# Performance work log

Hardware: AMD Instinct MI355X
Metric: run time of the kernel (lower is better)

## Reference

```python
import jax, jax.numpy as jnp
import numpy as np

B, SQ, ST, SI = 8, 4096, 77, 16
C, DC, H = 1280, 2048, 20
DH = C // H  # 64
SCALE = 1.0 / np.sqrt(DH).astype(np.float32)
SCALE_ID = 1.0
SCALE_HAIR = 1.0


def setup_inputs() -> dict:
    key = jax.random.key(0)
    ks = jax.random.split(key, 12)
    std = 0.02
    return {
        "hidden_states": jax.random.normal(ks[0], (B, SQ, C), jnp.float32),
        "text_states": jax.random.normal(ks[1], (B, ST, DC), jnp.float32),
        "id_states": jax.random.normal(ks[2], (B, SI, DC), jnp.float32),
        "hair_states": jax.random.normal(ks[3], (B, SI, DC), jnp.float32),
        # weights stored as [in, out] (transpose of torch nn.Linear layout)
        "Wq": jax.random.normal(ks[4], (C, C), jnp.float32) * std,
        "Wk": jax.random.normal(ks[5], (DC, C), jnp.float32) * std,
        "Wv": jax.random.normal(ks[6], (DC, C), jnp.float32) * std,
        "Wo": jax.random.normal(ks[7], (C, C), jnp.float32) * std,
        "b_o": jnp.zeros((C,), jnp.float32),
        "Wk_id": jax.random.normal(ks[8], (DC, C), jnp.float32) * std,
        "Wv_id": jax.random.normal(ks[9], (DC, C), jnp.float32) * std,
        "Wk_hair": jax.random.normal(ks[10], (DC, C), jnp.float32) * std,
        "Wv_hair": jax.random.normal(ks[11], (DC, C), jnp.float32) * std,
    }


def _heads(x):
    # [B, S, C] -> [B, H, S, DH]
    b, s, _ = x.shape
    return x.reshape(b, s, H, DH).transpose(0, 2, 1, 3)


def _merge(x):
    # [B, H, S, DH] -> [B, S, C]
    b, h, s, d = x.shape
    return x.transpose(0, 2, 1, 3).reshape(b, s, h * d)


def _attend(q, k, v):
    # q: [B,H,Sq,DH], k/v: [B,H,Sk,DH]; fp32 scores (attn_fp32=True)
    scores = jnp.einsum("bhqd,bhkd->bhqk", q.astype(jnp.float32), k.astype(jnp.float32)) * SCALE
    p = jax.nn.softmax(scores, axis=-1)
    return jnp.einsum("bhqk,bhkd->bhqd", p, v.astype(jnp.float32))


def reference(hidden_states, text_states, id_states, hair_states, Wq, Wk, Wv, Wo, b_o, Wk_id, Wv_id, Wk_hair, Wv_hair):
    q = _heads(hidden_states @ Wq)
    # base cross-attention to text (standard diffusers AttnProcessor)
    base = _attend(q, _heads(text_states @ Wk), _heads(text_states @ Wv))
    result = _merge(base) @ Wo + b_o
    # ID branch: own K/V projections, shared query and to_out
    out_id = _attend(q, _heads(id_states @ Wk_id), _heads(id_states @ Wv_id))
    result = result + SCALE_ID * (_merge(out_id) @ Wo + b_o)
    # hair branch
    out_h = _attend(q, _heads(hair_states @ Wk_hair), _heads(hair_states @ Wv_hair))
    result = result + SCALE_HAIR * (_merge(out_h) @ Wo + b_o)
    return result
```

## Files before the change

### kernel.cpp

```cpp
#include <hip/hip_runtime.h>
#include <cstdint>
#include <cstddef>

typedef unsigned short u16;
typedef __attribute__((ext_vector_type(4))) float     f32x4_t;
typedef __attribute__((ext_vector_type(8))) __bf16    bf16x8_t;
typedef __attribute__((ext_vector_type(8))) u16       u16x8_t;
typedef __attribute__((ext_vector_type(4))) u16       u16x4_t;
typedef __attribute__((ext_vector_type(4))) float     fvec4_t;

#define DEVI __device__ __forceinline__

constexpr int Bn  = 8;
constexpr int SQn = 4096;
constexpr int STn = 77;
constexpr int SIn = 16;
constexpr int Cn  = 1280;
constexpr int DCn = 2048;
constexpr int Hn  = 20;
constexpr float SCALEf = 0.125f;
constexpr float L2E    = 1.4426950408889634f;

typedef const __attribute__((address_space(1))) void* gas_t;
typedef __attribute__((address_space(3))) void*       las_t;

DEVI u16 f2bf(float f) {
  union { float f; unsigned u; } cv; cv.f = f;
  unsigned u = cv.u;
  return (u16)((u + 0x7FFFu + ((u >> 16) & 1u)) >> 16);
}

__global__ __launch_bounds__(256) void cast_bf16_kernel(
    const float* __restrict__ src, u16* __restrict__ dst, int n8) {
  int i = blockIdx.x * 256 + threadIdx.x;
  if (i >= n8) return;
  const fvec4_t* s4 = (const fvec4_t*)src;
  fvec4_t a = s4[2 * i], b = s4[2 * i + 1];
  u16x8_t o;
  o[0] = f2bf(a[0]); o[1] = f2bf(a[1]); o[2] = f2bf(a[2]); o[3] = f2bf(a[3]);
  o[4] = f2bf(b[0]); o[5] = f2bf(b[1]); o[6] = f2bf(b[2]); o[7] = f2bf(b[3]);
  ((u16x8_t*)dst)[i] = o;
}

struct TrArgs {
  const float* src[8];
  u16*         dst[8];
  int          Kd[8];
};

__global__ __launch_bounds__(256) void transpose_cast_kernel(TrArgs ta) {
  int z = blockIdx.z;
  int K = ta.Kd[z];
  int k0 = blockIdx.x * 32;
  if (k0 >= K) return;
  int n0 = blockIdx.y * 32;
  __shared__ float tile[32][33];
  int tx = threadIdx.x & 31, ty = threadIdx.x >> 5;
  const float* src = ta.src[z];
#pragma unroll
  for (int i = 0; i < 4; i++) {
    int r = ty + 8 * i;
    tile[r][tx] = src[(size_t)(k0 + r) * Cn + n0 + tx];
  }
  __syncthreads();
  u16* dst = ta.dst[z];
#pragma unroll
  for (int i = 0; i < 4; i++) {
    int r = ty + 8 * i;
    dst[(size_t)(n0 + r) * K + k0 + tx] = f2bf(tile[tx][r]);
  }
}

template <int OUT_MODE, int A_HM>
__global__ __launch_bounds__(512, 2) void gemm256_kernel(
    const u16* __restrict__ A, const u16* __restrict__ Bt,
    void* __restrict__ Cout, const float* __restrict__ bias, int M, int K) {
  __shared__ __align__(16) u16 lds[2][2][256 * 64];
  const int t = threadIdx.x;
  const int w = t >> 6, l = t & 63;
  const int wr = w >> 2, wc = w & 3;
  const int lr = l & 15;
  const int m0 = blockIdx.x * 256, n0 = blockIdx.y * 256;
  const int NT = K >> 6;

  f32x4_t acc[8][4];
#pragma unroll
  for (int am = 0; am < 8; am++)
#pragma unroll
    for (int an = 0; an < 4; an++) {
      f32x4_t z = {0.f, 0.f, 0.f, 0.f};
      acc[am][an] = z;
    }

  auto stagePart = [&](int cb, int kt, int i) {
    const int k0 = kt * 64;
    int row = i * 64 + w * 8 + (l >> 3);
    int col16 = (l & 7) ^ (row & 7);
    const u16* ga;
    if (A_HM) {
      int gr = m0 + row, bb = gr >> 12, ss = gr & 4095;
      ga = A + (((size_t)bb * Hn + kt) * SQn + ss) * 64 + col16 * 8;
    } else {
      ga = A + (size_t)(m0 + row) * K + k0 + col16 * 8;
    }
    __builtin_amdgcn_global_load_lds((gas_t)ga, (las_t)(&lds[cb][0][0] + (size_t)(i * 512 + w * 64) * 8), 16, 0, 0);
    const u16* gb = Bt + (size_t)(n0 + row) * K + k0 + col16 * 8;
    __builtin_amdgcn_global_load_lds((gas_t)gb, (las_t)(&lds[cb][1][0] + (size_t)(i * 512 + w * 64) * 8), 16, 0, 0);
  };
  auto readB = [&](bf16x8_t (&dst)[2][2], const u16* bB, int qn) {
#pragma unroll
    for (int n = 0; n < 2; n++) {
      int row = wc * 64 + qn * 32 + n * 16 + lr;
#pragma unroll
      for (int kk = 0; kk < 2; kk++) {
        int slot = kk * 4 + (l >> 4);
        dst[n][kk] = *(const bf16x8_t*)&bB[row * 64 + ((slot ^ (row & 7)) * 8)];
      }
    }
  };
  auto readA = [&](bf16x8_t (&dst)[4][2], const u16* bA, int qm) {
#pragma unroll
    for (int m = 0; m < 4; m++) {
      int row = wr * 128 + qm * 64 + m * 16 + lr;
#pragma unroll
      for (int kk = 0; kk < 2; kk++) {
        int slot = kk * 4 + (l >> 4);
        dst[m][kk] = *(const bf16x8_t*)&bA[row * 64 + ((slot ^ (row & 7)) * 8)];
      }
    }
  };
  auto mfma16 = [&](bf16x8_t (&Af)[4][2], bf16x8_t (&Bf)[2][2], int qm, int qn) {
    __builtin_amdgcn_s_setprio(1);
#pragma unroll
    for (int m = 0; m < 4; m++)
#pragma unroll
      for (int n = 0; n < 2; n++) {
        acc[qm * 4 + m][qn * 2 + n] = __builtin_amdgcn_mfma_f32_16x16x32_bf16(
            Af[m][0], Bf[n][0], acc[qm * 4 + m][qn * 2 + n], 0, 0, 0);
        acc[qm * 4 + m][qn * 2 + n] = __builtin_amdgcn_mfma_f32_16x16x32_bf16(
            Af[m][1], Bf[n][1], acc[qm * 4 + m][qn * 2 + n], 0, 0, 0);
      }
    __builtin_amdgcn_s_setprio(0);
  };

#pragma unroll
  for (int i = 0; i < 4; i++) stagePart(0, 0, i);
#pragma unroll
  for (int i = 0; i < 4; i++) stagePart(1, 1, i);
  asm volatile("s_waitcnt vmcnt(8)" ::: "memory");
  __builtin_amdgcn_sched_barrier(0);
  __builtin_amdgcn_s_barrier();

  for (int kt = 0; kt < NT; kt++) {
    const int cb = kt & 1;
    const u16* bA = &lds[cb][0][0];
    const u16* bB = &lds[cb][1][0];
    const bool st = (kt + 2 < NT);
    bf16x8_t Ar[4][2], B0[2][2], B1[2][2];

    readB(B0, bB, 0);
    readA(Ar, bA, 0);
    __builtin_amdgcn_s_barrier();
    asm volatile("s_waitcnt lgkmcnt(0)" ::: "memory");
    __builtin_amdgcn_sched_barrier(0);
    mfma16(Ar, B0, 0, 0);
    __builtin_amdgcn_s_barrier();

    readB(B1, bB, 1);
    __builtin_amdgcn_s_barrier();
    asm volatile("s_waitcnt lgkmcnt(0)" ::: "memory");
    __builtin_amdgcn_sched_barrier(0);
    mfma16(Ar, B1, 0, 1);
    __builtin_amdgcn_s_barrier();

    readA(Ar, bA, 1);
    __builtin_amdgcn_s_barrier();
    if (st) { stagePart(cb, kt + 2, 0); stagePart(cb, kt + 2, 1); }
    asm volatile("s_waitcnt lgkmcnt(0)" ::: "memory");
    __builtin_amdgcn_sched_barrier(0);
    mfma16(Ar, B0, 1, 0);
    __builtin_amdgcn_s_barrier();

    if (st) { stagePart(cb, kt + 2, 2); stagePart(cb, kt + 2, 3); }
    mfma16(Ar, B1, 1, 1);

    if (st) {
      asm volatile("s_waitcnt vmcnt(8)" ::: "memory");
    } else if (kt + 1 < NT) {
      asm volatile("s_waitcnt vmcnt(0)" ::: "memory");
    }
    __builtin_amdgcn_sched_barrier(0);
    __builtin_amdgcn_s_barrier();
  }

#pragma unroll
  for (int am = 0; am < 8; am++) {
    int rbase = m0 + wr * 128 + am * 16 + (l >> 4) * 4;
#pragma unroll
    for (int an = 0; an < 4; an++) {
      int col = n0 + wc * 64 + an * 16 + lr;
#pragma unroll
      for (int j = 0; j < 4; j++) {
        int r = rbase + j;
        if (OUT_MODE == 1) {
          ((float*)Cout)[(size_t)r * Cn + col] = acc[am][an][j] + 3.0f * bias[col];
        } else {
          int bb = r >> 12, ss = r & 4095;
          int hh = (n0 >> 6) + wc, dd = an * 16 + lr;
          ((u16*)Cout)[(((size_t)bb * Hn + hh) * SQn + ss) * 64 + dd] = f2bf(acc[am][an][j]);
        }
      }
    }
  }
}

DEVI void gemm_body(const u16* __restrict__ A, const u16* __restrict__ Bt,
                    u16* __restrict__ Cout, int M, int S, int K, int mtile, int ntile) {
  __shared__ __align__(16) u16 lA[128 * 64];
  __shared__ __align__(16) u16 lB[128 * 64];
  const int t = threadIdx.x;
  const int w = t >> 6, l = t & 63;
  const int wr = w >> 1, wc = w & 1;
  const int m0 = mtile * 128, n0 = ntile * 128;
  const int lr = l & 15, lk = (l >> 4) * 8;

  f32x4_t acc[4][4];
#pragma unroll
  for (int m = 0; m < 4; m++)
#pragma unroll
    for (int n = 0; n < 4; n++) {
      f32x4_t z = {0.f, 0.f, 0.f, 0.f};
      acc[m][n] = z;
    }

  for (int k0 = 0; k0 < K; k0 += 64) {
    __syncthreads();
#pragma unroll
    for (int i = 0; i < 4; i++) {
      int c = i * 256 + t;
      int row = c >> 3, ch = c & 7;
      int rA = m0 + row;
      rA = rA < M ? rA : M - 1;
      const u16* ga = A + (size_t)rA * K + k0 + ch * 8;
      __builtin_amdgcn_global_load_lds((gas_t)ga, (las_t)&lA[(i * 256 + w * 64) * 8], 16, 0, 0);
      const u16* gb = Bt + (size_t)(n0 + row) * K + k0 + ch * 8;
      __builtin_amdgcn_global_load_lds((gas_t)gb, (las_t)&lB[(i * 256 + w * 64) * 8], 16, 0, 0);
    }
    __syncthreads();
#pragma unroll
    for (int kk = 0; kk < 2; kk++) {
      bf16x8_t af[4], bf[4];
#pragma unroll
      for (int m = 0; m < 4; m++)
        af[m] = *(const bf16x8_t*)&lA[(64 * wr + 16 * m + lr) * 64 + kk * 32 + lk];
#pragma unroll
      for (int n = 0; n < 4; n++)
        bf[n] = *(const bf16x8_t*)&lB[(64 * wc + 16 * n + lr) * 64 + kk * 32 + lk];
#pragma unroll
      for (int m = 0; m < 4; m++)
#pragma unroll
        for (int n = 0; n < 4; n++)
          acc[m][n] = __builtin_amdgcn_mfma_f32_16x16x32_bf16(af[m], bf[n], acc[m][n], 0, 0, 0);
    }
  }

  const int rj = (l >> 4) * 4;
  const int hh = ntile * 2 + wc;
#pragma unroll
  for (int m = 0; m < 4; m++) {
    int rbase = m0 + 64 * wr + 16 * m + rj;
#pragma unroll
    for (int n = 0; n < 4; n++) {
      int dd = 16 * n + lr;
#pragma unroll
      for (int j = 0; j < 4; j++) {
        int r = rbase + j;
        if (r < M) {
          int bb = r / S, ss = r - bb * S;
          Cout[(((size_t)bb * Hn + hh) * S + ss) * 64 + dd] = f2bf(acc[m][n][j]);
        }
      }
    }
  }
}

struct KV6 {
  const u16* A[6];
  const u16* Bt[6];
  u16*       Cp[6];
  int        M[6];
  int        S[6];
};

__global__ __launch_bounds__(256) void gemm_kv_kernel(KV6 kv) {
  int z = blockIdx.z;
  int M = kv.M[z];
  if ((int)blockIdx.x * 128 >= M) return;
  gemm_body(kv.A[z], kv.Bt[z], kv.Cp[z], M, kv.S[z], DCn, blockIdx.x, blockIdx.y);
}

__global__ __launch_bounds__(256) void attn_kernel(
    const u16* __restrict__ q,
    const u16* __restrict__ ktx, const u16* __restrict__ vtx,
    const u16* __restrict__ kid, const u16* __restrict__ vid,
    const u16* __restrict__ kh,  const u16* __restrict__ vh,
    u16* __restrict__ osum) {
  __shared__ __align__(16) u16 KP[4 * 16 * 136];
  __shared__ __align__(16) u16 Vt[64 * 128];

  const int t = threadIdx.x, w = t >> 6, l = t & 63;
  const int bh = blockIdx.y;
  const int lr = l & 15, lk = (l >> 4) * 8;

  const u16* qB   = q   + ((size_t)bh) * SQn * 64;
  const u16* ktxB = ktx + ((size_t)bh) * STn * 64;
  const u16* vtxB = vtx + ((size_t)bh) * STn * 64;
  const u16* kidB = kid + ((size_t)bh) * SIn * 64;
  const u16* vidB = vid + ((size_t)bh) * SIn * 64;
  const u16* khB  = kh  + ((size_t)bh) * SIn * 64;
  const u16* vhB  = vh  + ((size_t)bh) * SIn * 64;
  u16*       oB   = osum + ((size_t)bh) * SQn * 64;

  for (int i = t; i < 112 * 8; i += 256) {
    int row = i >> 3, ch = i & 7;
    u16x8_t vv;
#pragma unroll
    for (int x = 0; x < 8; x++) vv[x] = 0;
    if (row < 77)
      vv = *(const u16x8_t*)(ktxB + (size_t)row * 64 + ch * 8);
    else if (row >= 80 && row < 96)
      vv = *(const u16x8_t*)(kidB + (size_t)(row - 80) * 64 + ch * 8);
    else if (row >= 96)
      vv = *(const u16x8_t*)(khB + (size_t)(row - 96) * 64 + ch * 8);
    *(u16x8_t*)&KP[row * 72 + ch * 8] = vv;
  }
  for (int i = t; i < 128 * 8; i += 256) {
    int key = i >> 3, ch = i & 7;
    u16x8_t vv;
#pragma unroll
    for (int x = 0; x < 8; x++) vv[x] = 0;
    if (key < 77)
      vv = *(const u16x8_t*)(vtxB + (size_t)key * 64 + ch * 8);
    else if (key >= 80 && key < 96)
      vv = *(const u16x8_t*)(vidB + (size_t)(key - 80) * 64 + ch * 8);
    else if (key >= 96 && key < 112)
      vv = *(const u16x8_t*)(vhB + (size_t)(key - 96) * 64 + ch * 8);
    int G = key >> 3, wk = key & 7;
#pragma unroll
    for (int x = 0; x < 8; x++) {
      int d = ch * 8 + x;
      int Gs = G ^ x ^ ch;
      Vt[d * 128 + Gs * 8 + wk] = vv[x];
    }
  }
  __syncthreads();

  bf16x8_t kf[7][2];
#pragma unroll
  for (int tt = 0; tt < 7; tt++)
#pragma unroll
    for (int kk = 0; kk < 2; kk++)
      kf[tt][kk] = *(const bf16x8_t*)&KP[(tt * 16 + lr) * 72 + kk * 32 + lk];
  __syncthreads();

  u16* Pw = &KP[w * 16 * 136];
  {
    u16x4_t z4; z4[0] = 0; z4[1] = 0; z4[2] = 0; z4[3] = 0;
    *(u16x4_t*)&Pw[(l >> 2) * 136 + 112 + (l & 3) * 4] = z4;
  }

  for (int rt = 0; rt < 4; rt++) {
    const int s0 = blockIdx.x * 256 + w * 64 + rt * 16;
    bf16x8_t qf[2];
#pragma unroll
    for (int kk = 0; kk < 2; kk++)
      qf[kk] = *(const bf16x8_t*)&qB[(size_t)(s0 + lr) * 64 + kk * 32 + lk];

    f32x4_t sc[7];
#pragma unroll
    for (int tt = 0; tt < 7; tt++) {
      f32x4_t z = {0.f, 0.f, 0.f, 0.f};
      z = __builtin_amdgcn_mfma_f32_16x16x32_bf16(qf[0], kf[tt][0], z, 0, 0, 0);
      z = __builtin_amdgcn_mfma_f32_16x16x32_bf16(qf[1], kf[tt][1], z, 0, 0, 0);
      sc[tt] = z;
    }
#pragma unroll
    for (int tt = 0; tt < 7; tt++)
#pragma unroll
      for (int j = 0; j < 4; j++) sc[tt][j] *= SCALEf;
    if (lr >= 13) {
#pragma unroll
      for (int j = 0; j < 4; j++) sc[4][j] = -3.0e38f;
    }

    float mx[4], sm[4], inv[4];

#pragma unroll
    for (int j = 0; j < 4; j++) {
      float m = sc[0][j];
      m = fmaxf(m, sc[1][j]); m = fmaxf(m, sc[2][j]);
      m = fmaxf(m, sc[3][j]); m = fmaxf(m, sc[4][j]);
      mx[j] = m;
    }
#pragma unroll
    for (int d = 1; d < 16; d <<= 1)
#pragma unroll
      for (int j = 0; j < 4; j++) mx[j] = fmaxf(mx[j], __shfl_xor(mx[j], d));
#pragma unroll
    for (int j = 0; j < 4; j++) sm[j] = 0.f;
#pragma unroll
    for (int tt = 0; tt < 5; tt++)
#pragma unroll
      for (int j = 0; j < 4; j++) {
        float p = __builtin_amdgcn_exp2f((sc[tt][j] - mx[j]) * L2E);
        sc[tt][j] = p;
        sm[j] += p;
      }
#pragma unroll
    for (int d = 1; d < 16; d <<= 1)
#pragma unroll
      for (int j = 0; j < 4; j++) sm[j] += __shfl_xor(sm[j], d);
#pragma unroll
    for (int j = 0; j < 4; j++) inv[j] = __builtin_amdgcn_rcpf(sm[j]);
#pragma unroll
    for (int tt = 0; tt < 5; tt++)
#pragma unroll
      for (int j = 0; j < 4; j++) {
        __bf16 pb = (__bf16)(sc[tt][j] * inv[j]);
        Pw[((l >> 4) * 4 + j) * 136 + tt * 16 + lr] = *(u16*)&pb;
      }

#pragma unroll
    for (int j = 0; j < 4; j++) mx[j] = sc[5][j];
#pragma unroll
    for (int d = 1; d < 16; d <<= 1)
#pragma unroll
      for (int j = 0; j < 4; j++) mx[j] = fmaxf(mx[j], __shfl_xor(mx[j], d));
#pragma unroll
    for (int j = 0; j < 4; j++) {
      float p = __builtin_amdgcn_exp2f((sc[5][j] - mx[j]) * L2E);
      sc[5][j] = p;
      sm[j] = p;
    }
#pragma unroll
    for (int d = 1; d < 16; d <<= 1)
#pragma unroll
      for (int j = 0; j < 4; j++) sm[j] += __shfl_xor(sm[j], d);
#pragma unroll
    for (int j = 0; j < 4; j++) {
      __bf16 pb = (__bf16)(sc[5][j] * __builtin_amdgcn_rcpf(sm[j]));
      Pw[((l >> 4) * 4 + j) * 136 + 80 + lr] = *(u16*)&pb;
    }

#pragma unroll
    for (int j = 0; j < 4; j++) mx[j] = sc[6][j];
#pragma unroll
    for (int d = 1; d < 16; d <<= 1)
#pragma unroll
      for (int j = 0; j < 4; j++) mx[j] = fmaxf(mx[j], __shfl_xor(mx[j], d));
#pragma unroll
    for (int j = 0; j < 4; j++) {
      float p = __builtin_amdgcn_exp2f((sc[6][j] - mx[j]) * L2E);
      sc[6][j] = p;
      sm[j] = p;
    }
#pragma unroll
    for (int d = 1; d < 16; d <<= 1)
#pragma unroll
      for (int j = 0; j < 4; j++) sm[j] += __shfl_xor(sm[j], d);
#pragma unroll
    for (int j = 0; j < 4; j++) {
      __bf16 pb = (__bf16)(sc[6][j] * __builtin_amdgcn_rcpf(sm[j]));
      Pw[((l >> 4) * 4 + j) * 136 + 96 + lr] = *(u16*)&pb;
    }

    f32x4_t oacc[4];
#pragma unroll
    for (int n = 0; n < 4; n++) {
      f32x4_t z = {0.f, 0.f, 0.f, 0.f};
      oacc[n] = z;
    }
#pragma unroll
    for (int ktile = 0; ktile < 4; ktile++) {
      bf16x8_t pf = *(const bf16x8_t*)&Pw[lr * 136 + ktile * 32 + lk];
#pragma unroll
      for (int n = 0; n < 4; n++) {
        int d = 16 * n + lr;
        int Gs = (4 * ktile + (l >> 4)) ^ (d & 7) ^ ((d >> 3) & 7);
        bf16x8_t vf = *(const bf16x8_t*)&Vt[d * 128 + Gs * 8];
        oacc[n] = __builtin_amdgcn_mfma_f32_16x16x32_bf16(pf, vf, oacc[n], 0, 0, 0);
      }
    }
#pragma unroll
    for (int n = 0; n < 4; n++)
#pragma unroll
      for (int j = 0; j < 4; j++) {
        int srow = s0 + (l >> 4) * 4 + j;
        __bf16 ob = (__bf16)oacc[n][j];
        oB[(size_t)srow * 64 + 16 * n + lr] = *(u16*)&ob;
      }
  }
}

extern "C" void kernel_launch(void* const* d_in, const int* in_sizes, int n_in,
                              void* d_out, int out_size, void* d_ws, size_t ws_size,
                              hipStream_t stream) {
  (void)in_sizes; (void)n_in; (void)out_size; (void)ws_size;
  const float* hidden  = (const float*)d_in[0];
  const float* text    = (const float*)d_in[1];
  const float* ids     = (const float*)d_in[2];
  const float* hair    = (const float*)d_in[3];
  const float* Wq      = (const float*)d_in[4];
  const float* Wk      = (const float*)d_in[5];
  const float* Wv      = (const float*)d_in[6];
  const float* Wo      = (const float*)d_in[7];
  const float* b_o     = (const float*)d_in[8];
  const float* Wk_id   = (const float*)d_in[9];
  const float* Wv_id   = (const float*)d_in[10];
  const float* Wk_hair = (const float*)d_in[11];
  const float* Wv_hair = (const float*)d_in[12];
  float* out = (float*)d_out;

  char* ws = (char*)d_ws;
  size_t off = 0;
  auto carve = [&](size_t bytes) -> char* {
    char* p = ws + off;
    off += (bytes + 255) & ~(size_t)255;
    return p;
  };

  u16* h_bf    = (u16*)carve((size_t)Bn * SQn * Cn * 2);
  u16* q_bf    = (u16*)carve((size_t)Bn * SQn * Cn * 2);
  u16* text_bf = (u16*)carve((size_t)Bn * STn * DCn * 2);
  u16* id_bf   = (u16*)carve((size_t)Bn * SIn * DCn * 2);
  u16* hair_bf = (u16*)carve((size_t)Bn * SIn * DCn * 2);
  u16* Wq_t    = (u16*)carve((size_t)Cn * Cn * 2);
  u16* Wo_t    = (u16*)carve((size_t)Cn * Cn * 2);
  u16* Wk_t    = (u16*)carve((size_t)DCn * Cn * 2);
  u16* Wv_t    = (u16*)carve((size_t)DCn * Cn * 2);
  u16* Wkid_t  = (u16*)carve((size_t)DCn * Cn * 2);
  u16* Wvid_t  = (u16*)carve((size_t)DCn * Cn * 2);
  u16* Wkh_t   = (u16*)carve((size_t)DCn * Cn * 2);
  u16* Wvh_t   = (u16*)carve((size_t)DCn * Cn * 2);
  u16* k_text  = (u16*)carve((size_t)Bn * STn * Cn * 2);
  u16* v_text  = (u16*)carve((size_t)Bn * STn * Cn * 2);
  u16* k_id    = (u16*)carve((size_t)Bn * SIn * Cn * 2);
  u16* v_id    = (u16*)carve((size_t)Bn * SIn * Cn * 2);
  u16* k_hr    = (u16*)carve((size_t)Bn * SIn * Cn * 2);
  u16* v_hr    = (u16*)carve((size_t)Bn * SIn * Cn * 2);
  u16* attn_sum = h_bf;

  {
    int n8 = Bn * SQn * Cn / 8;
    cast_bf16_kernel<<<dim3((n8 + 255) / 256), 256, 0, stream>>>(hidden, h_bf, n8);
  }
  {
    int n8 = Bn * STn * DCn / 8;
    cast_bf16_kernel<<<dim3((n8 + 255) / 256), 256, 0, stream>>>(text, text_bf, n8);
  }
  {
    int n8 = Bn * SIn * DCn / 8;
    cast_bf16_kernel<<<dim3((n8 + 255) / 256), 256, 0, stream>>>(ids, id_bf, n8);
    cast_bf16_kernel<<<dim3((n8 + 255) / 256), 256, 0, stream>>>(hair, hair_bf, n8);
  }

  {
    TrArgs ta;
    ta.src[0] = Wq;      ta.dst[0] = Wq_t;   ta.Kd[0] = Cn;
    ta.src[1] = Wo;      ta.dst[1] = Wo_t;   ta.Kd[1] = Cn;
    ta.src[2] = Wk;      ta.dst[2] = Wk_t;   ta.Kd[2] = DCn;
    ta.src[3] = Wv;      ta.dst[3] = Wv_t;   ta.Kd[3] = DCn;
    ta.src[4] = Wk_id;   ta.dst[4] = Wkid_t; ta.Kd[4] = DCn;
    ta.src[5] = Wv_id;   ta.dst[5] = Wvid_t; ta.Kd[5] = DCn;
    ta.src[6] = Wk_hair; ta.dst[6] = Wkh_t;  ta.Kd[6] = DCn;
    ta.src[7] = Wv_hair; ta.dst[7] = Wvh_t;  ta.Kd[7] = DCn;
    transpose_cast_kernel<<<dim3(DCn / 32, Cn / 32, 8), 256, 0, stream>>>(ta);
  }

  gemm256_kernel<2, 0><<<dim3(Bn * SQn / 256, Cn / 256), 512, 0, stream>>>(
      h_bf, Wq_t, q_bf, nullptr, Bn * SQn, Cn);

  {
    KV6 kv;
    kv.A[0] = text_bf; kv.Bt[0] = Wk_t;   kv.Cp[0] = k_text; kv.M[0] = Bn * STn; kv.S[0] = STn;
    kv.A[1] = text_bf; kv.Bt[1] = Wv_t;   kv.Cp[1] = v_text; kv.M[1] = Bn * STn; kv.S[1] = STn;
    kv.A[2] = id_bf;   kv.Bt[2] = Wkid_t; kv.Cp[2] = k_id;   kv.M[2] = Bn * SIn; kv.S[2] = SIn;
    kv.A[3] = id_bf;   kv.Bt[3] = Wvid_t; kv.Cp[3] = v_id;   kv.M[3] = Bn * SIn; kv.S[3] = SIn;
    kv.A[4] = hair_bf; kv.Bt[4] = Wkh_t;  kv.Cp[4] = k_hr;   kv.M[4] = Bn * SIn; kv.S[4] = SIn;
    kv.A[5] = hair_bf; kv.Bt[5] = Wvh_t;  kv.Cp[5] = v_hr;   kv.M[5] = Bn * SIn; kv.S[5] = SIn;
    gemm_kv_kernel<<<dim3((Bn * STn + 127) / 128, Cn / 128, 6), 256, 0, stream>>>(kv);
  }

  attn_kernel<<<dim3(SQn / 256, Bn * Hn), 256, 0, stream>>>(
      q_bf, k_text, v_text, k_id, v_id, k_hr, v_hr, attn_sum);

  gemm256_kernel<1, 1><<<dim3(Bn * SQn / 256, Cn / 256), 512, 0, stream>>>(
      attn_sum, Wo_t, out, b_o, Bn * SQn, Cn);
}
```

Baseline: 490.0 us.

## Reorder GEMM inner loop by K-halves and drop most workgroup barriers

```diff
diff --git a/kernel.cpp b/kernel.cpp
--- a/kernel.cpp
+++ b/kernel.cpp
@@ -107,39 +107,29 @@
     const u16* gb = Bt + (size_t)(n0 + row) * K + k0 + col16 * 8;
     __builtin_amdgcn_global_load_lds((gas_t)gb, (las_t)(&lds[cb][1][0] + (size_t)(i * 512 + w * 64) * 8), 16, 0, 0);
   };
-  auto readB = [&](bf16x8_t (&dst)[2][2], const u16* bB, int qn) {
-#pragma unroll
-    for (int n = 0; n < 2; n++) {
-      int row = wc * 64 + qn * 32 + n * 16 + lr;
-#pragma unroll
-      for (int kk = 0; kk < 2; kk++) {
-        int slot = kk * 4 + (l >> 4);
-        dst[n][kk] = *(const bf16x8_t*)&bB[row * 64 + ((slot ^ (row & 7)) * 8)];
-      }
+  auto readA8 = [&](bf16x8_t (&dst)[8], const u16* bA, int kh) {
+#pragma unroll
+    for (int m = 0; m < 8; m++) {
+      int row = wr * 128 + m * 16 + lr;
+      int slot = kh * 4 + (l >> 4);
+      dst[m] = *(const bf16x8_t*)&bA[row * 64 + ((slot ^ (row & 7)) * 8)];
     }
   };
-  auto readA = [&](bf16x8_t (&dst)[4][2], const u16* bA, int qm) {
-#pragma unroll
-    for (int m = 0; m < 4; m++) {
-      int row = wr * 128 + qm * 64 + m * 16 + lr;
-#pragma unroll
-      for (int kk = 0; kk < 2; kk++) {
-        int slot = kk * 4 + (l >> 4);
-        dst[m][kk] = *(const bf16x8_t*)&bA[row * 64 + ((slot ^ (row & 7)) * 8)];
-      }
+  auto readB4 = [&](bf16x8_t (&dst)[4], const u16* bB, int kh) {
+#pragma unroll
+    for (int n = 0; n < 4; n++) {
+      int row = wc * 64 + n * 16 + lr;
+      int slot = kh * 4 + (l >> 4);
+      dst[n] = *(const bf16x8_t*)&bB[row * 64 + ((slot ^ (row & 7)) * 8)];
     }
   };
-  auto mfma16 = [&](bf16x8_t (&Af)[4][2], bf16x8_t (&Bf)[2][2], int qm, int qn) {
+  auto mfma32 = [&](bf16x8_t (&Af)[8], bf16x8_t (&Bf)[4]) {
     __builtin_amdgcn_s_setprio(1);
 #pragma unroll
-    for (int m = 0; m < 4; m++)
-#pragma unroll
-      for (int n = 0; n < 2; n++) {
-        acc[qm * 4 + m][qn * 2 + n] = __builtin_amdgcn_mfma_f32_16x16x32_bf16(
-            Af[m][0], Bf[n][0], acc[qm * 4 + m][qn * 2 + n], 0, 0, 0);
-        acc[qm * 4 + m][qn * 2 + n] = __builtin_amdgcn_mfma_f32_16x16x32_bf16(
-            Af[m][1], Bf[n][1], acc[qm * 4 + m][qn * 2 + n], 0, 0, 0);
-      }
+    for (int m = 0; m < 8; m++)
+#pragma unroll
+      for (int n = 0; n < 4; n++)
+        acc[m][n] = __builtin_amdgcn_mfma_f32_16x16x32_bf16(Af[m], Bf[n], acc[m][n], 0, 0, 0);
     __builtin_amdgcn_s_setprio(0);
   };
 
@@ -156,33 +146,24 @@
     const u16* bA = &lds[cb][0][0];
     const u16* bB = &lds[cb][1][0];
     const bool st = (kt + 2 < NT);
-    bf16x8_t Ar[4][2], B0[2][2], B1[2][2];
-
-    readB(B0, bB, 0);
-    readA(Ar, bA, 0);
-    __builtin_amdgcn_s_barrier();
+    bf16x8_t Af[8], Bf[4];
+
+    readA8(Af, bA, 0);
+    readB4(Bf, bB, 0);
     asm volatile("s_waitcnt lgkmcnt(0)" ::: "memory");
     __builtin_amdgcn_sched_barrier(0);
-    mfma16(Ar, B0, 0, 0);
+    mfma32(Af, Bf);
+
+    readA8(Af, bA, 1);
+    readB4(Bf, bB, 1);
     __builtin_amdgcn_s_barrier();
-
-    readB(B1, bB, 1);
-    __builtin_amdgcn_s_barrier();
+    if (st) {
+      stagePart(cb, kt + 2, 0); stagePart(cb, kt + 2, 1);
+      stagePart(cb, kt + 2, 2); stagePart(cb, kt + 2, 3);
+    }
     asm volatile("s_waitcnt lgkmcnt(0)" ::: "memory");
     __builtin_amdgcn_sched_barrier(0);
-    mfma16(Ar, B1, 0, 1);
-    __builtin_amdgcn_s_barrier();
-
-    readA(Ar, bA, 1);
-    __builtin_amdgcn_s_barrier();
-    if (st) { stagePart(cb, kt + 2, 0); stagePart(cb, kt + 2, 1); }
-    asm volatile("s_waitcnt lgkmcnt(0)" ::: "memory");
-    __builtin_amdgcn_sched_barrier(0);
-    mfma16(Ar, B0, 1, 0);
-    __builtin_amdgcn_s_barrier();
-
-    if (st) { stagePart(cb, kt + 2, 2); stagePart(cb, kt + 2, 3); }
-    mfma16(Ar, B1, 1, 1);
+    mfma32(Af, Bf);
 
     if (st) {
       asm volatile("s_waitcnt vmcnt(8)" ::: "memory");
```

Result: no change. 482.4 us (-1.6%).
